# Optimization experiments

Hardware: AMD Instinct MI355X
Metric: run time of the kernel (lower is better)

## Reference

```python
import jax, jax.numpy as jnp
import numpy as np

N = 100_000      # nodes
E = 800_000      # edges per edge type
T = 3            # num_edge_types - 1 relation-specific convs
D_IN = 128
D_OUT = 128


def setup_inputs() -> dict:
    key = jax.random.key(0)
    k1, k2, k3, k4 = jax.random.split(key, 4)
    x = jax.random.normal(k1, (N, D_IN), dtype=jnp.float32)
    edges = jax.random.randint(k2, (T, 2, E), 0, N, dtype=jnp.int32)
    W = jax.random.normal(k3, (T, D_IN, D_OUT), dtype=jnp.float32) * (1.0 / np.sqrt(D_IN))
    b = jax.random.normal(k4, (T, D_OUT), dtype=jnp.float32) * 0.02
    return {"x": x, "edges": edges, "W": W, "b": b}


def _gcn_conv(x, ei, W, b):
    """PyG GCNConv: add self-loops, symmetric D^-1/2 (A+I) D^-1/2 norm, XW, +b."""
    n = x.shape[0]
    xw = x @ W                                   # [N, D_OUT]
    loop = jnp.arange(n, dtype=ei.dtype)
    src = jnp.concatenate([ei[0], loop])         # [E+N]
    dst = jnp.concatenate([ei[1], loop])         # [E+N]
    deg = jax.ops.segment_sum(jnp.ones(src.shape[0], xw.dtype), dst, num_segments=n)
    dis = jnp.where(deg > 0, jax.lax.rsqrt(jnp.maximum(deg, 1e-12)), 0.0)
    norm = dis[src] * dis[dst]                   # [E+N]
    msg = xw[src] * norm[:, None]                # gather-transform: [E+N, D_OUT]
    out = jax.ops.segment_sum(msg, dst, num_segments=n)  # scatter-add back to nodes
    return out + b


def reference(x, edges, W, b):
    # Sum of per-edge-type GCN convolutions into a shared output buffer.
    out = jnp.zeros((x.shape[0], W.shape[-1]), dtype=x.dtype)
    for i in range(edges.shape[0]):              # small fixed relation loop
        out = out + _gcn_conv(x, edges[i], W[i], b[i])
    return out
```

## Files before the change

kernel.cpp:

```cpp
#include <hip/hip_runtime.h>

#define NN 100000
#define EE 800000
#define TT 3
#define D  128
#define NB 391
#define CAPB 7168
#define CHUNK 4096
#define LSTRIDE 392

typedef unsigned short bf16_t;

typedef __bf16 bf16x8_t __attribute__((ext_vector_type(8)));
typedef float  f32x4_t  __attribute__((ext_vector_type(4)));

union ABFrag { bf16x8_t v; uint4 q; };

__device__ __forceinline__ bf16_t f2bf(float f) {
    unsigned u = __float_as_uint(f);
    u += 0x7fff + ((u >> 16) & 1);
    return (bf16_t)(u >> 16);
}
__device__ __forceinline__ float bf_lo(unsigned p) { return __uint_as_float(p << 16); }
__device__ __forceinline__ float bf_hi(unsigned p) { return __uint_as_float(p & 0xFFFF0000u); }

__global__ void quant_kernel(const float* __restrict__ x, bf16_t* __restrict__ xq) {
    int i = (blockIdx.x * 256 + threadIdx.x) * 4;
    if (i >= NN * D) return;
    float4 f = *(const float4*)(x + i);
    uint2 p;
    p.x = (unsigned)f2bf(f.x) | ((unsigned)f2bf(f.y) << 16);
    p.y = (unsigned)f2bf(f.z) | ((unsigned)f2bf(f.w) << 16);
    *(uint2*)(xq + i) = p;
}

__global__ void wconv_kernel(const float* __restrict__ W, bf16_t* __restrict__ WT) {
    int t = blockIdx.y, n = blockIdx.x, k = threadIdx.x;
    WT[((size_t)t * D + n) * D + k] = f2bf(W[((size_t)t * D + k) * D + n]);
}

__global__ __launch_bounds__(256) void bin_kernel(const int* __restrict__ edges,
                                                  int* __restrict__ bcnt,
                                                  unsigned* __restrict__ bin) {
    __shared__ int hist[NB];
    __shared__ int gbase[NB];
    int tid = threadIdx.x;
    int t = blockIdx.y;
    int f0 = blockIdx.x * CHUNK;
    const int* sb = edges + (size_t)t * 2 * EE;
    const int* db = sb + EE;

    for (int i = tid; i < NB; i += 256) hist[i] = 0;
    __syncthreads();

    int4 s4[4], d4[4];
    int rank[16];
    bool have[4];
#pragma unroll
    for (int j = 0; j < 4; ++j) {
        int e = f0 + ((j * 256 + tid) << 2);
        have[j] = (e < EE);
        if (have[j]) { s4[j] = *(const int4*)(sb + e); d4[j] = *(const int4*)(db + e); }
    }
#pragma unroll
    for (int j = 0; j < 4; ++j) {
        if (have[j]) {
            int dd0 = d4[j].x, dd1 = d4[j].y, dd2 = d4[j].z, dd3 = d4[j].w;
            rank[j * 4 + 0] = atomicAdd(&hist[dd0 >> 8], 1);
            rank[j * 4 + 1] = atomicAdd(&hist[dd1 >> 8], 1);
            rank[j * 4 + 2] = atomicAdd(&hist[dd2 >> 8], 1);
            rank[j * 4 + 3] = atomicAdd(&hist[dd3 >> 8], 1);
        }
    }
    __syncthreads();
    for (int i = tid; i < NB; i += 256) {
        int h = hist[i];
        gbase[i] = (h > 0) ? atomicAdd(&bcnt[i], h) : 0;
    }
    __syncthreads();
#pragma unroll
    for (int j = 0; j < 4; ++j) {
        if (have[j]) {
            int ss[4] = {s4[j].x, s4[j].y, s4[j].z, s4[j].w};
            int dd[4] = {d4[j].x, d4[j].y, d4[j].z, d4[j].w};
#pragma unroll
            for (int k = 0; k < 4; ++k) {
                int bkt = dd[k] >> 8;
                int pb = gbase[bkt] + rank[j * 4 + k];
                if (pb < CAPB)
                    bin[(size_t)bkt * CAPB + pb] =
                        ((unsigned)(dd[k] & 255) << 19) | ((unsigned)t << 17) | (unsigned)ss[k];
            }
        }
    }
}

#define MAXR 14
__global__ __launch_bounds__(512) void sort_kernel(const int* __restrict__ bcnt,
                                                   unsigned* __restrict__ bin,
                                                   float* __restrict__ dis3,
                                                   int* __restrict__ cnts3,
                                                   int* __restrict__ nodeoff) {
    __shared__ int cnt[768];
    __shared__ int tot[256];
    int tid = threadIdx.x;
    int b = blockIdx.x;
    int c = bcnt[b]; if (c > CAPB) c = CAPB;
    unsigned* reg = bin + (size_t)b * CAPB;

    for (int i = tid; i < 768; i += 512) cnt[i] = 0;
    __syncthreads();

    unsigned ur[MAXR];
    int rr[MAXR];
    bool vld[MAXR];
#pragma unroll
    for (int k = 0; k < MAXR; ++k) {
        int i = tid + k * 512;
        vld[k] = (i < c);
        unsigned u = vld[k] ? reg[i] : 0u;
        ur[k] = u;
        int bi = (int)(u >> 19) * 3 + (int)((u >> 17) & 3);
        rr[k] = vld[k] ? atomicAdd(&cnt[bi], 1) : 0;
    }
    __syncthreads();

    int d0 = 0, d1 = 0, d2 = 0;
    if (tid < 256) {
        d0 = cnt[tid * 3]; d1 = cnt[tid * 3 + 1]; d2 = cnt[tid * 3 + 2];
        tot[tid] = d0 + d1 + d2;
    }
    __syncthreads();
    for (int off = 1; off < 256; off <<= 1) {
        int v = 0;
        if (tid < 256 && tid >= off) v = tot[tid - off];
        __syncthreads();
        if (tid < 256 && tid >= off) tot[tid] += v;
        __syncthreads();
    }
    if (tid < 256) {
        int excl = tot[tid] - (d0 + d1 + d2);
        int gnode = b * 256 + tid;
        if (gnode < NN) {
            nodeoff[gnode] = b * CAPB + excl;
            cnts3[gnode]   = d0 | (d1 << 8) | (d2 << 16);
            dis3[gnode]            = rsqrtf((float)d0 + 1.f);
            dis3[NN + gnode]       = rsqrtf((float)d1 + 1.f);
            dis3[2 * NN + gnode]   = rsqrtf((float)d2 + 1.f);
        }
        cnt[tid * 3]     = excl;
        cnt[tid * 3 + 1] = excl + d0;
        cnt[tid * 3 + 2] = excl + d0 + d1;
    }
    __syncthreads();
#pragma unroll
    for (int k = 0; k < MAXR; ++k) {
        if (vld[k]) {
            unsigned u = ur[k];
            int bi = (int)(u >> 19) * 3 + (int)((u >> 17) & 3);
            reg[cnt[bi] + rr[k]] = u & 0x1FFFFu;
        }
    }
}


#define ISSUE(UX, WA, J0)                                                          \
    {                                                                              \
        const int _j0 = (J0);                                                      \
        _Pragma("unroll")                                                          \
        for (int k = 0; k < 8; ++k) {                                              \
            int sxk = __builtin_amdgcn_readlane(vsrc, _j0 + k);                    \
            int wbk = __builtin_amdgcn_readlane(wbits, _j0 + k);                   \
            WA[k] = (_j0 + k < cS) ? __int_as_float(wbk) : 0.0f;                   \
            UX[k] = *(const unsigned*)(xq + (size_t)sxk * D + (lane << 1));        \
        }                                                                          \
    }

#define CONSUME(UX, WA, J0)                                                        \
    {                                                                              \
        const int _j0 = (J0);                                                      \
        _Pragma("unroll")                                                          \
        for (int k = 0; k < 8; ++k) {                                              \
            int idxk = _j0 + k;                                                    \
            float wk = WA[k];                                                      \
            unsigned u = UX[k];                                                    \
            float xl = bf_lo(u), xh = bf_hi(u);                                    \
            if (idxk < b1S)      { a00 += wk * xl; a01 += wk * xh; }               \
            else if (idxk < b2S) { a10 += wk * xl; a11 += wk * xh; }               \
            else                 { a20 += wk * xl; a21 += wk * xh; }               \
        }                                                                          \
    }

__global__ __launch_bounds__(1024, 8) void fused_kernel(const bf16_t* __restrict__ xq,
                                                        const float* __restrict__ dis3,
                                                        const int* __restrict__ cnts3,
                                                        const int* __restrict__ nodeoff,
                                                        const unsigned* __restrict__ recs,
                                                        const bf16_t* __restrict__ WT,
                                                        const float* __restrict__ bias,
                                                        float* __restrict__ out) {
    __shared__ __attribute__((aligned(16))) ushort ylds[16 * LSTRIDE];
    int tid  = threadIdx.x;
    int lane = tid & 63;
    int wave = tid >> 6;
    int n0 = blockIdx.x * 16;
    int n  = n0 + wave;

    unsigned su = *(const unsigned*)(xq + (size_t)n * D + (lane << 1));
    float xs0 = bf_lo(su), xs1 = bf_hi(su);

    float dn0 = dis3[n], dn1 = dis3[NN + n], dn2 = dis3[2 * NN + n];
    int pk = cnts3[n];
    int d0 = pk & 255, d1 = (pk >> 8) & 255, d2 = (pk >> 16) & 255;
    int s0 = nodeoff[n];

    int b1S = __builtin_amdgcn_readfirstlane(d0);
    int b2S = __builtin_amdgcn_readfirstlane(d0 + d1);
    int cT  = d0 + d1 + d2; if (cT > 64) cT = 64;
    int cS  = __builtin_amdgcn_readfirstlane(cT);

    unsigned u = recs[s0 + (lane < cS ? lane : 0)];
    int tl = (lane < b1S) ? 0 : (lane < b2S) ? 1 : 2;
    int vsrc = (lane < cS) ? (int)(u & 0x1FFFFu) : 0;
    float ws = dis3[tl * NN + vsrc];
    int wbits = __float_as_int(ws);

    float a00 = dn0 * xs0, a01 = dn0 * xs1;
    float a10 = dn1 * xs0, a11 = dn1 * xs1;
    float a20 = dn2 * xs0, a21 = dn2 * xs1;

    unsigned uxA[8], uxB[8];
    float wA[8], wB[8];

    if (cS > 0) {
        int nb = (cS + 7) >> 3;
        ISSUE(uxA, wA, 0)
        int blk = 0;
        while (true) {
            if (blk + 1 < nb) ISSUE(uxB, wB, (blk + 1) * 8)
            CONSUME(uxA, wA, blk * 8)
            if (++blk >= nb) break;
            if (blk + 1 < nb) ISSUE(uxA, wA, (blk + 1) * 8)
            CONSUME(uxB, wB, blk * 8)
            if (++blk >= nb) break;
        }
    }

    {
        a00 *= dn0; a01 *= dn0; a10 *= dn1; a11 *= dn1; a20 *= dn2; a21 *= dn2;
        ushort* yw = ylds + wave * LSTRIDE + (lane << 1);
        *(unsigned*)(yw)         = (unsigned)f2bf(a00) | ((unsigned)f2bf(a01) << 16);
        *(unsigned*)(yw + D)     = (unsigned)f2bf(a10) | ((unsigned)f2bf(a11) << 16);
        *(unsigned*)(yw + 2 * D) = (unsigned)f2bf(a20) | ((unsigned)f2bf(a21) << 16);
    }
    __syncthreads();

    if (wave < 8) {
        int quad = lane >> 4;
        int lid  = lane & 15;
        int col  = wave * 16 + lid;
        f32x4_t acc = {0.f, 0.f, 0.f, 0.f};
        const ushort* yr = ylds + lid * LSTRIDE;
#pragma unroll
        for (int t = 0; t < TT; ++t) {
            const bf16_t* wn = WT + ((size_t)t * D + col) * D;
#pragma unroll
            for (int s = 0; s < 4; ++s) {
                ABFrag av, bv;
                av.q = *(const uint4*)(yr + t * D + s * 32 + quad * 8);
                bv.q = *(const uint4*)(wn + s * 32 + quad * 8);
                acc = __builtin_amdgcn_mfma_f32_16x16x32_bf16(av.v, bv.v, acc, 0, 0, 0);
            }
        }
        float bc = bias[col] + bias[D + col] + bias[2 * D + col];
#pragma unroll
        for (int r = 0; r < 4; ++r)
            out[(size_t)(n0 + quad * 4 + r) * D + col] = acc[r] + bc;
    }
}

extern "C" void kernel_launch(void* const* d_in, const int* in_sizes, int n_in,
                              void* d_out, int out_size, void* d_ws, size_t ws_size,
                              hipStream_t stream) {
    const float* x     = (const float*)d_in[0];
    const int*   edges = (const int*)d_in[1];
    const float* W     = (const float*)d_in[2];
    const float* b     = (const float*)d_in[3];
    float*       out   = (float*)d_out;

    char* w = (char*)d_ws;
    bf16_t*   xq      = (bf16_t*)w;
    unsigned* bin     = (unsigned*)(w + (size_t)NN * D * 2);
    float*    dis3    = (float*)((char*)bin + (size_t)NB * CAPB * 4);
    int*      cnts3   = (int*)((char*)dis3 + (size_t)3 * NN * 4);
    int*      nodeoff = cnts3 + NN;
    bf16_t*   WT      = (bf16_t*)(nodeoff + NN);
    int*      bcnt    = (int*)((char*)WT + (size_t)TT * D * D * 2);

    hipMemsetAsync(bcnt, 0, (size_t)NB * sizeof(int), stream);

    quant_kernel<<<(NN * D / 4 + 255) / 256, 256, 0, stream>>>(x, xq);
    {
        dim3 g(D, TT);
        wconv_kernel<<<g, D, 0, stream>>>(W, WT);
    }

    {
        dim3 g((EE + CHUNK - 1) / CHUNK, TT);
        bin_kernel<<<g, 256, 0, stream>>>(edges, bcnt, bin);
    }

    sort_kernel<<<NB, 512, 0, stream>>>(bcnt, bin, dis3, cnts3, nodeoff);

    fused_kernel<<<NN / 16, 1024, 0, stream>>>(xq, dis3, cnts3, nodeoff, bin, WT, b, out);
}
```

Measured before the change: 320.6 us.

## Stage binned edge records in shared memory for coalesced bucket writes

The bin kernel now uses 512 threads and runs a block-level prefix scan over bucket histograms. It stages each record and its global target in LDS ordered by bucket, then writes to global memory in a contiguous per-bucket order instead of scattering each edge directly. This should give more contiguous stores at the cost of an extra LDS pass, a 9-step scan with barriers, and about 36KB of LDS, which can limit occupancy. The fused kernel also drops per-element lane-bound checks: weights of inactive lanes are zeroed once, and records are read unconditionally with the source index clamped.

```diff
diff --git a/kernel.cpp b/kernel.cpp
--- a/kernel.cpp
+++ b/kernel.cpp
@@ -39,59 +39,82 @@
     WT[((size_t)t * D + n) * D + k] = f2bf(W[((size_t)t * D + k) * D + n]);
 }
 
-__global__ __launch_bounds__(256) void bin_kernel(const int* __restrict__ edges,
-                                                  int* __restrict__ bcnt,
-                                                  unsigned* __restrict__ bin) {
+__global__ __launch_bounds__(512, 8) void bin_kernel(const int* __restrict__ edges,
+                                                     int* __restrict__ bcnt,
+                                                     unsigned* __restrict__ bin) {
     __shared__ int hist[NB];
+    __shared__ int lbase[NB];
     __shared__ int gbase[NB];
+    __shared__ int scn[512];
+    __shared__ unsigned srec[CHUNK];
+    __shared__ unsigned stgt[CHUNK];
     int tid = threadIdx.x;
     int t = blockIdx.y;
     int f0 = blockIdx.x * CHUNK;
     const int* sb = edges + (size_t)t * 2 * EE;
     const int* db = sb + EE;
 
-    for (int i = tid; i < NB; i += 256) hist[i] = 0;
-    __syncthreads();
-
-    int4 s4[4], d4[4];
-    int rank[16];
-    bool have[4];
-#pragma unroll
-    for (int j = 0; j < 4; ++j) {
-        int e = f0 + ((j * 256 + tid) << 2);
+    for (int i = tid; i < NB; i += 512) hist[i] = 0;
+    __syncthreads();
+
+    int4 s4[2], d4[2];
+    int rnk[8];
+    bool have[2];
+#pragma unroll
+    for (int j = 0; j < 2; ++j) {
+        int e = f0 + ((j * 512 + tid) << 2);
         have[j] = (e < EE);
         if (have[j]) { s4[j] = *(const int4*)(sb + e); d4[j] = *(const int4*)(db + e); }
     }
 #pragma unroll
-    for (int j = 0; j < 4; ++j) {
+    for (int j = 0; j < 2; ++j) {
         if (have[j]) {
-            int dd0 = d4[j].x, dd1 = d4[j].y, dd2 = d4[j].z, dd3 = d4[j].w;
-            rank[j * 4 + 0] = atomicAdd(&hist[dd0 >> 8], 1);
-            rank[j * 4 + 1] = atomicAdd(&hist[dd1 >> 8], 1);
-            rank[j * 4 + 2] = atomicAdd(&hist[dd2 >> 8], 1);
-            rank[j * 4 + 3] = atomicAdd(&hist[dd3 >> 8], 1);
-        }
-    }
-    __syncthreads();
-    for (int i = tid; i < NB; i += 256) {
-        int h = hist[i];
-        gbase[i] = (h > 0) ? atomicAdd(&bcnt[i], h) : 0;
-    }
-    __syncthreads();
-#pragma unroll
-    for (int j = 0; j < 4; ++j) {
+            rnk[j * 4 + 0] = atomicAdd(&hist[d4[j].x >> 8], 1);
+            rnk[j * 4 + 1] = atomicAdd(&hist[d4[j].y >> 8], 1);
+            rnk[j * 4 + 2] = atomicAdd(&hist[d4[j].z >> 8], 1);
+            rnk[j * 4 + 3] = atomicAdd(&hist[d4[j].w >> 8], 1);
+        }
+    }
+    __syncthreads();
+
+    int hv = (tid < NB) ? hist[tid] : 0;
+    scn[tid] = hv;
+    __syncthreads();
+    for (int off = 1; off < 512; off <<= 1) {
+        int u = 0;
+        if (tid >= off) u = scn[tid - off];
+        __syncthreads();
+        if (tid >= off) scn[tid] += u;
+        __syncthreads();
+    }
+    if (tid < NB) {
+        lbase[tid] = scn[tid] - hv;
+        gbase[tid] = (hv > 0) ? atomicAdd(&bcnt[tid], hv) : 0;
+    }
+    __syncthreads();
+
+#pragma unroll
+    for (int j = 0; j < 2; ++j) {
         if (have[j]) {
             int ss[4] = {s4[j].x, s4[j].y, s4[j].z, s4[j].w};
             int dd[4] = {d4[j].x, d4[j].y, d4[j].z, d4[j].w};
 #pragma unroll
             for (int k = 0; k < 4; ++k) {
                 int bkt = dd[k] >> 8;
-                int pb = gbase[bkt] + rank[j * 4 + k];
-                if (pb < CAPB)
-                    bin[(size_t)bkt * CAPB + pb] =
-                        ((unsigned)(dd[k] & 255) << 19) | ((unsigned)t << 17) | (unsigned)ss[k];
+                int r = rnk[j * 4 + k];
+                int pos = lbase[bkt] + r;
+                int rel = gbase[bkt] + r;
+                srec[pos] = ((unsigned)(dd[k] & 255) << 19) | ((unsigned)t << 17) | (unsigned)ss[k];
+                stgt[pos] = (rel < CAPB) ? (unsigned)(bkt * CAPB + rel) : 0xFFFFFFFFu;
             }
         }
+    }
+    __syncthreads();
+
+    int nval = EE - f0; if (nval > CHUNK) nval = CHUNK;
+    for (int i = tid; i < nval; i += 512) {
+        unsigned tg = stgt[i];
+        if (tg != 0xFFFFFFFFu) bin[tg] = srec[i];
     }
 }
 
@@ -171,7 +194,7 @@
         for (int k = 0; k < 8; ++k) {                                              \
             int sxk = __builtin_amdgcn_readlane(vsrc, _j0 + k);                    \
             int wbk = __builtin_amdgcn_readlane(wbits, _j0 + k);                   \
-            WA[k] = (_j0 + k < cS) ? __int_as_float(wbk) : 0.0f;                   \
+            WA[k] = __int_as_float(wbk);                                           \
             UX[k] = *(const unsigned*)(xq + (size_t)sxk * D + (lane << 1));        \
         }                                                                          \
     }
@@ -219,10 +242,12 @@
     int cT  = d0 + d1 + d2; if (cT > 64) cT = 64;
     int cS  = __builtin_amdgcn_readfirstlane(cT);
 
-    unsigned u = recs[s0 + (lane < cS ? lane : 0)];
+    unsigned u = recs[s0 + lane];
     int tl = (lane < b1S) ? 0 : (lane < b2S) ? 1 : 2;
-    int vsrc = (lane < cS) ? (int)(u & 0x1FFFFu) : 0;
-    float ws = dis3[tl * NN + vsrc];
+    int vsrc = (int)(u & 0x1FFFFu);
+    if (vsrc >= NN) vsrc = 0;
+    float ws = 0.0f;
+    if (lane < cS) ws = dis3[tl * NN + vsrc];
     int wbits = __float_as_int(ws);
 
     float a00 = dn0 * xs0, a01 = dn0 * xs1;
@@ -307,7 +332,7 @@
 
     {
         dim3 g((EE + CHUNK - 1) / CHUNK, TT);
-        bin_kernel<<<g, 256, 0, stream>>>(edges, bcnt, bin);
+        bin_kernel<<<g, 512, 0, stream>>>(edges, bcnt, bin);
     }
 
     sort_kernel<<<NB, 512, 0, stream>>>(bcnt, bin, dis3, cnts3, nodeoff);
```

Result: faster. 308.9 us (-3.6%).
